# Performance work log

Measured on AMD Instinct MI355X. Metric: run time of the kernel, lower is better.

Reference implementation:

```python
import jax, jax.numpy as jnp
import numpy as np

B, N, E = 16, 512, 131072
FEAT, EMB, H = 3, 512, 3
K1, K2 = 410, 205  # ceil(0.8*512), ceil(0.5*410) per PyG TopKPooling
NEG_SLOPE, EPS = 0.2, 1e-5


def _gat_conv(x, W, att_s, att_d, bias, src, tgt, valid, num_nodes):
    # PyG GATConv (concat=True): per-edge attention with segment softmax over targets.
    Hh, C = att_s.shape
    xp = (x @ W).reshape(-1, Hh, C)                      # [Nn,H,C]
    a_s = jnp.einsum('nhc,hc->nh', xp, att_s)
    a_d = jnp.einsum('nhc,hc->nh', xp, att_d)
    srcc = jnp.where(valid, src, 0)
    tgtc = jnp.where(valid, tgt, 0)
    e = jax.nn.leaky_relu(a_s[srcc] + a_d[tgtc], NEG_SLOPE)  # [Ee,H]
    seg = jnp.where(valid, tgt, num_nodes)               # invalid edges -> dummy segment
    emax = jax.ops.segment_max(e, seg, num_segments=num_nodes + 1)
    emax = jnp.where(jnp.isfinite(emax), emax, 0.0)
    ex = jnp.exp(e - emax[seg]) * valid[:, None].astype(e.dtype)
    den = jax.ops.segment_sum(ex, seg, num_segments=num_nodes + 1)
    alpha = ex / jnp.maximum(den[seg], 1e-16)            # [Ee,H]
    out = jax.ops.segment_sum(alpha[:, :, None] * xp[srcc], seg,
                              num_segments=num_nodes + 1)[:num_nodes]
    return out.reshape(num_nodes, Hh * C) + bias


def _bn(x, g, b):
    # BatchNorm1d, training-mode batch statistics (biased var), eps=1e-5
    m = x.mean(0)
    v = x.var(0)
    return (x - m) * jax.lax.rsqrt(v + EPS) * g + b


def _topk_pool(x, p, nb, n_per, k):
    # PyG TopKPooling: score = tanh(x.w/||w||), keep top-k per graph, scale by score
    score = jnp.tanh((x @ p) / jnp.linalg.norm(p))       # [nb*n_per]
    top_s, top_i = jax.lax.top_k(score.reshape(nb, n_per), k)
    perm = (top_i + jnp.arange(nb)[:, None] * n_per).reshape(-1)
    x_new = x[perm] * top_s.reshape(-1, 1)
    mapping = jnp.full((nb * n_per,), -1, jnp.int32).at[perm].set(
        jnp.arange(nb * k, dtype=jnp.int32))
    return x_new, mapping


def _pool_cat(x, nb, k):
    # [global_max_pool, global_mean_pool] over equal-size graphs
    xr = x.reshape(nb, k, -1)
    return jnp.concatenate([xr.max(1), xr.mean(1)], axis=1)


def _forward(x, W1, as1, ad1, bc1, Wh1, bh1, g1, be1, p1,
             W2, as2, ad2, bc2, Wh2, bh2, g2, be2, p2,
             Wl1, bl1, Wl2, bl2, edge_index):
    Nn = B * N
    src0, tgt0 = edge_index[0], edge_index[1]
    sl = jnp.arange(Nn, dtype=jnp.int32)                 # GATConv add_self_loops=True
    src1 = jnp.concatenate([src0, sl]); tgt1 = jnp.concatenate([tgt0, sl])
    valid1 = jnp.ones(src1.shape, bool)
    h = _gat_conv(x, W1, as1, ad1, bc1, src1, tgt1, valid1, Nn)
    h = jax.nn.relu(h @ Wh1 + bh1)
    h = _bn(h, g1, be1)
    h, mapping = _topk_pool(h, p1, B, N, K1)
    x1 = _pool_cat(h, B, K1)                             # [B, 2*EMB]
    # relabel edges to pooled node ids; drop edges with removed endpoints via mask
    s2 = mapping[src0]; t2 = mapping[tgt0]
    v2 = (s2 >= 0) & (t2 >= 0)
    sl2 = jnp.arange(B * K1, dtype=jnp.int32)
    src2 = jnp.concatenate([s2, sl2]); tgt2 = jnp.concatenate([t2, sl2])
    valid2 = jnp.concatenate([v2, jnp.ones(sl2.shape, bool)])
    h = _gat_conv(h, W2, as2, ad2, bc2, src2, tgt2, valid2, B * K1)
    h = jax.nn.relu(h @ Wh2 + bh2)
    h = _bn(h, g2, be2)
    h, _ = _topk_pool(h, p2, B, K1, K2)
    x2 = _pool_cat(h, B, K2)
    xg = x1 + x2
    xg = jax.nn.relu(xg @ Wl1 + bl1)                     # dropout p=0.5 disabled (eval)
    return xg @ Wl2 + bl2                                # [B, 256]


def setup_inputs() -> dict:
    key = jax.random.key(0)
    ks = jax.random.split(key, 16)
    x = jax.random.normal(ks[0], (B * N, FEAT), jnp.float32)
    goff = jnp.repeat(jnp.arange(B, dtype=jnp.int32), E // B) * N
    src = jax.random.randint(ks[1], (E,), 0, N, jnp.int32) + goff
    tgt = jax.random.randint(ks[2], (E,), 0, N, jnp.int32) + goff
    edge_index = jnp.stack([src, tgt])
    s = 0.05
    p = {
        'W1': jax.random.normal(ks[3], (FEAT, H * EMB)) * s,
        'as1': jax.random.normal(ks[4], (H, EMB)) * s,
        'ad1': jax.random.normal(ks[5], (H, EMB)) * s,
        'bc1': jnp.zeros((H * EMB,)),
        'Wh1': jax.random.normal(ks[6], (H * EMB, EMB)) * s,
        'bh1': jnp.zeros((EMB,)),
        'g1': jnp.ones((EMB,)), 'be1': jnp.zeros((EMB,)),
        'p1': jax.random.normal(ks[7], (EMB,)) * s,
        'W2': jax.random.normal(ks[8], (EMB, H * EMB)) * s,
        'as2': jax.random.normal(ks[9], (H, EMB)) * s,
        'ad2': jax.random.normal(ks[10], (H, EMB)) * s,
        'bc2': jnp.zeros((H * EMB,)),
        'Wh2': jax.random.normal(ks[11], (H * EMB, EMB)) * s,
        'bh2': jnp.zeros((EMB,)),
        'g2': jnp.ones((EMB,)), 'be2': jnp.zeros((EMB,)),
        'p2': jax.random.normal(ks[12], (EMB,)) * s,
        'Wl1': jax.random.normal(ks[13], (2 * EMB, 512)) * s,
        'bl1': jnp.zeros((512,)),
        'Wl2': jax.random.normal(ks[14], (512, 256)) * s,
        'bl2': jnp.zeros((256,)),
    }
    return {'x': x, 'edge_index': edge_index, **p}


def reference(x, edge_index, W1, as1, ad1, bc1, Wh1, bh1, g1, be1, p1,
              W2, as2, ad2, bc2, Wh2, bh2, g2, be2, p2, Wl1, bl1, Wl2, bl2):
    return _forward(x, W1, as1, ad1, bc1, Wh1, bh1, g1, be1, p1,
                    W2, as2, ad2, bc2, Wh2, bh2, g2, be2, p2,
                    Wl1, bl1, Wl2, bl2, edge_index)
```

## Files before the change

kernel.cpp:

```cpp
#include <hip/hip_runtime.h>
#include <hip/hip_bf16.h>
#include <math.h>

#define E_EDGES 131072
#define NN1 8192
#define NN2 6560
#define NG 16
#define NP1 512
#define KP1 410
#define KP2 205
#define F1 1536
#define EMB 512
#define MAXDEG 256
#define BNCH 256

typedef __hip_bfloat16 bf16;
typedef __attribute__((ext_vector_type(8))) short short8;
typedef __attribute__((ext_vector_type(4))) float f32x4;
typedef __attribute__((ext_vector_type(4))) unsigned short us4;

__device__ inline float wred64(float v){
  #pragma unroll
  for (int o = 32; o; o >>= 1) v += __shfl_down(v, o);
  return v;
}
__device__ inline float b2f_raw(unsigned short u){
  return __uint_as_float((unsigned)u << 16);
}
union BFU { bf16 b; unsigned short u; };
// ... 4 lines not shown
      (const __attribute__((address_space(1))) void*)g,
      (__attribute__((address_space(3))) void*)l, 16, 0, 0);
}

__device__ inline void split_store(float v, bf16* __restrict__ ph, bf16* __restrict__ pl){
  bf16 hi = __float2bfloat16(v);
  *ph = hi;
  *pl = __float2bfloat16(v - __bfloat162float(hi));
}

__device__ inline void bn_from_acc(const float* __restrict__ bnacc, int c, float fM,
                                   float& mean, float& inv){
  mean = bnacc[c] / fM;
  float var = fmaxf(bnacc[512+c]/fM - mean*mean, 0.f);
  inv = 1.f / sqrtf(var + 1e-5f);
}

__global__ __launch_bounds__(256) void k_pre(
    const float* __restrict__ W1, const float* __restrict__ as1, const float* __restrict__ ad1,
    const float* __restrict__ Wh1, const float* __restrict__ bc1, const float* __restrict__ bh1,
    const float* __restrict__ W2, const float* __restrict__ as2, const float* __restrict__ ad2,
    const float* __restrict__ Wh2, const float* __restrict__ bc2, const float* __restrict__ bh2,
    float* __restrict__ was1, float* __restrict__ wad1, float* __restrict__ M1p,
    float* __restrict__ cvp,
    float* __restrict__ was2, float* __restrict__ wad2,
    int* __restrict__ cnt1, int* __restrict__ cnt2, int* __restrict__ map,
    float* __restrict__ bnacc, float* __restrict__ bnacc1){
  int b = blockIdx.x, t = threadIdx.x;
  if (b < 24){
    int h = b / 8, rem = b % 8, jh = rem >> 2, kc = rem & 3;
    int j = jh*256 + t, c0 = kc*128;
    __shared__ float w1s[3][128];
    for (int i = t; i < 384; i += 256)
      w1s[i>>7][i&127] = W1[(i>>7)*1536 + h*512 + c0 + (i&127)];
    __syncthreads();
    const float* whc = Wh1 + (size_t)(h*512 + c0)*512 + j;
    float a0=0.f, a1=0.f, a2=0.f;
    #pragma unroll 8
    for (int c = 0; c < 128; c++){
      float v = whc[(size_t)c*512];
      a0 += w1s[0][c]*v; a1 += w1s[1][c]*v; a2 += w1s[2][c]*v;
    }
// ... 29 lines not shown
      float d = v0.x*a[0]+v0.y*a[1]+v0.z*a[2]+v0.w*a[3]
              + v1.x*a[4]+v1.y*a[5]+v1.z*a[6]+v1.w*a[7];
      d = wred64(d);
      if (lane == 0) (kind ? wad2 : was2)[h*512 + e] = d;
    }
  } else if (b < 170){
    if (t < 64){
      int bb = b - 152;
      int kind = bb / 9, r = bb % 9, h = r / 3, f = r % 3;
      const float* att = kind ? ad1 : as1;
      float s = 0.f;
      for (int c = t; c < 512; c += 64) s += W1[f*1536 + h*512 + c] * att[h*512 + c];
      s = wred64(s);
      if (t == 0) (kind ? wad1 : was1)[h*3 + f] = s;
    }
  } else {
    int i = (b - 170)*256 + t;
    if (i < NN1){ cnt1[i] = 1; map[i] = -1; }
    if (i < NN2){ cnt2[i] = 1; }
    if (i < 1024){ bnacc[i] = 0.f; bnacc1[i] = 0.f; }
  }
}

__global__ __launch_bounds__(256) void k_gemm_s_c1(const float* __restrict__ A0,
    const float* __restrict__ B0, bf16* __restrict__ Th, bf16* __restrict__ Tl,
    const int* __restrict__ tgt0, int* __restrict__ cnt1){
  int b = blockIdx.x;
  if (b >= 192){
    int i = (b - 192)*256 + threadIdx.x;
    if (i < E_EDGES) atomicAdd(&cnt1[tgt0[i]], 1);
    return;
  }
  int z = b % 3; int rr = b / 3; int by = rr >> 3, bx = rr & 7;
  const float* A = A0 + (size_t)z*512;
  const float* B = B0 + (size_t)z*512*512;
  __shared__ __align__(16) short sAh[4096], sAl[4096], sBh[4096], sBl[4096];
  int t = threadIdx.x, w = t >> 6, lane = t & 63;
  int l16 = lane & 15, q = lane >> 4;
  int bm = by*64, bn = bx*64;

  int am  = t >> 2, akw = (t & 3)*16;
  int bnl = t & 63, bkq = (t >> 6)*16;

  f32x4 acc[4];
  #pragma unroll
  for (int nf = 0; nf < 4; nf++) acc[nf] = (f32x4){0.f,0.f,0.f,0.f};

  float va[16], vb[16];
  #define GS_LOAD(K0) do { \
    _Pragma("unroll") for (int u = 0; u < 4; u++){ \
      float4 v4 = *(const float4*)(A + (size_t)(bm+am)*1536 + (K0) + akw + u*4); \
      va[u*4]=v4.x; va[u*4+1]=v4.y; va[u*4+2]=v4.z; va[u*4+3]=v4.w; } \
    _Pragma("unroll") for (int u = 0; u < 16; u++) \
      vb[u] = B[(size_t)((K0) + bkq + u)*512 + bn + bnl]; \
  } while(0)

  GS_LOAD(0);
  for (int it = 0; it < 8; it++){
    #pragma unroll
    for (int hh = 0; hh < 2; hh++){
      short8 ah_, al_, bh_, bl_;
      #pragma unroll
      for (int jj = 0; jj < 8; jj++){
        float v = va[hh*8+jj];
        unsigned short hu = f2u(v);
        ah_[jj] = (short)hu; al_[jj] = (short)f2u(v - b2f_raw(hu));
        v = vb[hh*8+jj];
        hu = f2u(v);
        bh_[jj] = (short)hu; bl_[jj] = (short)f2u(v - b2f_raw(hu));
      }
      int aoff = am*64  + ((((akw>>3) + hh) ^ (am  & 7)) << 3);
      *(short8*)(sAh + aoff) = ah_;
      *(short8*)(sAl + aoff) = al_;
      int boff = bnl*64 + ((((bkq>>3) + hh) ^ (bnl & 7)) << 3);
      *(short8*)(sBh + boff) = bh_;
      *(short8*)(sBl + boff) = bl_;
    }
    __syncthreads();
    if (it < 7) GS_LOAD((it+1)*64);
    #pragma unroll
    for (int ks = 0; ks < 2; ks++){
      int gc = ks*4 + q;
      int ar = w*16 + l16;
      int ao = ar*64 + ((gc ^ (ar & 7)) << 3);
      short8 afh = *(const short8*)(sAh + ao);
      short8 afl = *(const short8*)(sAl + ao);
      #pragma unroll
      for (int nf = 0; nf < 4; nf++){
        int br = nf*16 + l16;
        int bo = br*64 + ((gc ^ (br & 7)) << 3);
        short8 bfh = *(const short8*)(sBh + bo);
        short8 bfl = *(const short8*)(sBl + bo);
        acc[nf] = __builtin_amdgcn_mfma_f32_16x16x32_bf16(afh, bfh, acc[nf], 0, 0, 0);
        acc[nf] = __builtin_amdgcn_mfma_f32_16x16x32_bf16(afh, bfl, acc[nf], 0, 0, 0);
        acc[nf] = __builtin_amdgcn_mfma_f32_16x16x32_bf16(afl, bfh, acc[nf], 0, 0, 0);
      }
    }
    __syncthreads();
  }
  #undef GS_LOAD

  int m0 = bm + w*16 + q*4;
  #pragma unroll
  for (int nf = 0; nf < 4; nf++){
    int n = bn + nf*16 + l16;
    size_t base = (size_t)n*1536 + (size_t)z*512 + m0;
    #pragma unroll
    for (int e = 0; e < 4; e++)
      split_store(acc[nf][e], &Th[base+e], &Tl[base+e]);
  }
}

__device__ inline void scan_body(const int* __restrict__ counts, int* __restrict__ off,
                                 int* __restrict__ cur, int n, int* __restrict__ sh){
  int t = threadIdx.x;
  int chunk = (n + 1023) >> 10;
  int b = t * chunk; int e = b + chunk; if (e > n) e = n;
  int s = 0;
  for (int i = b; i < e; i++) s += counts[i];
  sh[t] = s; __syncthreads();
  for (int o = 1; o < 1024; o <<= 1){
    int v = (t >= o) ? sh[t-o] : 0;
    __syncthreads();
    sh[t] += v;
    __syncthreads();
  }
  int run = (t > 0) ? sh[t-1] : 0;
  for (int i = b; i < e; i++){ int c = counts[i]; off[i] = run; cur[i] = run; run += c; }
  if (t == 1023) off[n] = sh[1023];
}
__global__ __launch_bounds__(1024) void k_scan(const int* __restrict__ counts,
    int* __restrict__ off, int* __restrict__ cur, int n){
  __shared__ int sh[1024];
  scan_body(counts, off, cur, n, sh);
}
__global__ void k_fill1(const int* __restrict__ src0, const int* __restrict__ tgt0,
                        int* __restrict__ cur, int* __restrict__ esrc, int E, int nn){
  int i = blockIdx.x*blockDim.x + threadIdx.x;
  if (i >= E + nn) return;
  int s, tg;
  if (i < E){ s = src0[i]; tg = tgt0[i]; } else { s = i - E; tg = s; }
  int pos = atomicAdd(&cur[tg], 1);
  esrc[pos] = s;
}
__global__ void k_fill2(const int* __restrict__ src0, const int* __restrict__ tgt0,
                        const int* __restrict__ map, int* __restrict__ cur,
                        int* __restrict__ esrc, int E, int nn){
  int i = blockIdx.x*blockDim.x + threadIdx.x;
  if (i >= E + nn) return;
  int s, tg;
  if (i < E){
    s = map[src0[i]]; tg = map[tgt0[i]];
    if (s < 0 || tg < 0) return;
  } else { s = i - E; tg = s; }
  int pos = atomicAdd(&cur[tg], 1);
  esrc[pos] = s;
}

__global__ __launch_bounds__(64) void k_agg1(
    const float* __restrict__ x, const int* __restrict__ off, const int* __restrict__ esrc,
    const float* __restrict__ was, const float* __restrict__ wad,
    float* __restrict__ aggx){
  int n = blockIdx.x, t = threadIdx.x;
  __shared__ float xs[MAXDEG][3];
  __shared__ float al[MAXDEG*3];
  __shared__ float mh[3], dh[3];
  int s0 = off[n]; int deg = off[n+1] - s0; if (deg > MAXDEG) deg = MAXDEG;
  float ad0, ad1, ad2;
  {
    float x0 = x[n*3], x1 = x[n*3+1], x2 = x[n*3+2];
    ad0 = x0*wad[0] + x1*wad[1] + x2*wad[2];
    ad1 = x0*wad[3] + x1*wad[4] + x2*wad[5];
    ad2 = x0*wad[6] + x1*wad[7] + x2*wad[8];
  }
  for (int e = t; e < deg; e += 64){
    int s = esrc[s0 + e];
    float x0 = x[s*3], x1 = x[s*3+1], x2 = x[s*3+2];
    xs[e][0] = x0; xs[e][1] = x1; xs[e][2] = x2;
    float v0 = x0*was[0] + x1*was[1] + x2*was[2] + ad0;
    float v1 = x0*was[3] + x1*was[4] + x2*was[5] + ad1;
    float v2 = x0*was[6] + x1*was[7] + x2*was[8] + ad2;
    al[e*3+0] = v0 > 0.f ? v0 : 0.2f*v0;
    al[e*3+1] = v1 > 0.f ? v1 : 0.2f*v1;
    al[e*3+2] = v2 > 0.f ? v2 : 0.2f*v2;
  }
  __syncthreads();
  if (t < 3){
    float m = -INFINITY;
    for (int e = 0; e < deg; e++) m = fmaxf(m, al[e*3+t]);
    float d = 0.f;
    for (int e = 0; e < deg; e++) d += expf(al[e*3+t] - m);
    mh[t] = m; dh[t] = 1.f / fmaxf(d, 1e-16f);
  }
  __syncthreads();
  float acc[9] = {0,0,0,0,0,0,0,0,0};
  for (int e = t; e < deg; e += 64){
    #pragma unroll
    for (int h = 0; h < 3; h++){
      float a = expf(al[e*3+h] - mh[h]) * dh[h];
      acc[h*3+0] += a * xs[e][0];
      acc[h*3+1] += a * xs[e][1];
      acc[h*3+2] += a * xs[e][2];
    }
  }
  #pragma unroll
  for (int q = 0; q < 9; q++){
    float v = wred64(acc[q]);
    if (t == 0) aggx[(size_t)n*9 + q] = v;
  }
}

__global__ __launch_bounds__(256) void k_h1(const float* __restrict__ aggx,
    const float* __restrict__ M1p, const float* __restrict__ cvp1, bf16* __restrict__ hout,
    float* __restrict__ bnacc1){
  __shared__ float sM[9*512];
  __shared__ float sC[512];
  __shared__ float sA[32*9];
  int t = threadIdx.x; int n0 = blockIdx.x*32;
  for (int i = t; i < 9*512; i += 256)
    sM[i] = M1p[i] + M1p[4608 + i] + M1p[2*4608 + i] + M1p[3*4608 + i];
  for (int i = t; i < 512; i += 256){
    float s = 0.f;
    #pragma unroll
    for (int kc = 0; kc < 8; kc++) s += cvp1[kc*512 + i];
    sC[i] = s;
  }
  for (int i = t; i < 288; i += 256) sA[i] = aggx[(size_t)n0*9 + i];
  __syncthreads();
  float c0v = sC[t], c1v = sC[t+256];
  float ls0=0.f, lq0=0.f, ls1=0.f, lq1=0.f;
  #pragma unroll 4
  for (int i = 0; i < 32; i++){
    float a0 = c0v, a1 = c1v;
    #pragma unroll
    for (int q = 0; q < 9; q++){
      float av = sA[i*9+q];
      a0 += av * sM[q*512 + t];
      a1 += av * sM[q*512 + t + 256];
    }
    a0 = fmaxf(a0, 0.f); a1 = fmaxf(a1, 0.f);
    hout[(size_t)(n0+i)*512 + t]       = __float2bfloat16(a0);
    hout[(size_t)(n0+i)*512 + t + 256] = __float2bfloat16(a1);
    ls0 += a0; lq0 += a0*a0; ls1 += a1; lq1 += a1*a1;
  }
  atomicAdd(&bnacc1[t],           ls0);
  atomicAdd(&bnacc1[t+256],       ls1);
  atomicAdd(&bnacc1[512 + t],     lq0);
  atomicAdd(&bnacc1[512 + t+256], lq1);
}

__global__ __launch_bounds__(256) void k_score(
    const bf16* __restrict__ h, const float* __restrict__ bnacc, int M,
    const float* __restrict__ g_, const float* __restrict__ be,
    const float* __restrict__ p, float* __restrict__ score){
  int r = blockIdx.x, t = threadIdx.x;
  float fM = (float)M;
  float dot = 0.f, pp = 0.f;
  #pragma unroll
  for (int k = 0; k < 2; k++){
    int c = t + k*256;
    float mean, inv; bn_from_acc(bnacc, c, fM, mean, inv);
    float v = (__bfloat162float(h[(size_t)r*EMB + c]) - mean) * inv * g_[c] + be[c];
    float pc = p[c];
    dot += v * pc;
    pp += pc * pc;
  }
  dot = wred64(dot); pp = wred64(pp);
  __shared__ float red[4], redp[4];
  int lane = t & 63, wv = t >> 6;
  if (lane == 0){ red[wv] = dot; redp[wv] = pp; }
  __syncthreads();
  if (t == 0){
    float d = red[0]+red[1]+red[2]+red[3];
    float pn = sqrtf(redp[0]+redp[1]+redp[2]+redp[3]);
    score[r] = tanhf(d / pn);
  }
}

__global__ __launch_bounds__(512) void k_topk_sort(
    const float* __restrict__ score, int* __restrict__ map,
    int* __restrict__ topi, float* __restrict__ tops, int n_per, int K){
  int g = blockIdx.x, t = threadIdx.x;
  __shared__ float sk[512];
  __shared__ int si[512];
  if (t < n_per){ sk[t] = score[g*n_per + t]; si[t] = t; }
  else { sk[t] = -INFINITY; si[t] = 0x7fffffff; }
  __syncthreads();
  for (int k = 2; k <= 512; k <<= 1){
    for (int j = k >> 1; j > 0; j >>= 1){
      int l = t ^ j;
      if (l > t){
        float ki = sk[t], kl = sk[l]; int ii = si[t], il = si[l];
        bool before_l = (kl > ki) || (kl == ki && il < ii);
        bool up = ((t & k) == 0);
        if (up == before_l){ sk[t]=kl; sk[l]=ki; si[t]=il; si[l]=ii; }
      }
      __syncthreads();
    }
  }
  if (t < K){
    if (map) map[g*n_per + si[t]] = g*K + t;
// ... 41 lines not shown
      a[hh]   = v0*was2[hh*512 + c0] + v1*was2[hh*512 + c1];
      a[3+hh] = v0*wad2[hh*512 + c0] + v1*wad2[hh*512 + c1];
    }
    __shared__ float red[6][4];
    int lane = t & 63, wv = t >> 6;
    #pragma unroll
    for (int q = 0; q < 6; q++){ float v = wred64(a[q]); if (lane==0) red[q][wv]=v; }
    __syncthreads();
    if (t < 6){
      float sm = red[t][0]+red[t][1]+red[t][2]+red[t][3];
      if (t < 3) aso[row*3+t] = sm; else ado[row*3+(t-3)] = sm;
    }
  }
}

__global__ __launch_bounds__(1024) void k_poolA_scan(const bf16* __restrict__ xn,
    float* __restrict__ cat, int K,
    const int* __restrict__ cnt2, int* __restrict__ off2, int* __restrict__ cur2){
  __shared__ int shi[1024];
  __shared__ float smax[8][128];
  __shared__ float ssum[8][128];
  int b = blockIdx.x, t = threadIdx.x;
  if (b == 64){ scan_body(cnt2, off2, cur2, NN2, shi); return; }
  int g = b >> 2, cb = b & 3;
  int c = t & 127, rg = t >> 7;
  int col = cb*128 + c;
  const unsigned short* p = (const unsigned short*)xn + (size_t)g*K*EMB + col;
  float mx = -INFINITY, sm = 0.f;
  for (int r = rg; r < K; r += 8){
    float v = b2f_raw(p[(size_t)r*EMB]);
// ... 90 lines not shown
  #pragma unroll
  for (int k = 0; k < 2; k++){
    int c = t + k*256;
    #pragma unroll
    for (int h = 0; h < 3; h++)
      oh[(size_t)n*1536 + h*512 + c] = __float2bfloat16(acc[k][h]);
  }
}

__global__ __launch_bounds__(256, 2) void k_gemm_mfma(
    const bf16* __restrict__ Ah,
    const bf16* __restrict__ Bh, const bf16* __restrict__ Bl,
    const float* __restrict__ bias, bf16* __restrict__ C,
    float* __restrict__ bnacc,
    int M, int N, int K, int Mtiles){
  __shared__ __align__(16) unsigned short lds[2][16384];
  int t = threadIdx.x, w = t >> 6, lane = t & 63;
  int q = lane >> 4, l16 = lane & 15;
  int bmi = (int)blockIdx.x % Mtiles, bni = (int)blockIdx.x / Mtiles;
  int bm = bmi * 128, bn = bni * 64;

  int lr = lane >> 3, lc = lane & 7;
  int kg = ((lc ^ lr) & 7) * 8;
  int ro = w*8 + lr;
  int m0 = bm + ro, m1 = bm + 32 + ro, m2 = bm + 64 + ro, m3 = bm + 96 + ro;
  if (m0 >= M) m0 = M-1;  if (m1 >= M) m1 = M-1;
  if (m2 >= M) m2 = M-1;  if (m3 >= M) m3 = M-1;
  int n0 = bn + ro, n1 = bn + 32 + ro;
  const bf16* ptr[8];
  ptr[0] = Ah + (size_t)m0*K + kg;
  ptr[1] = Ah + (size_t)m1*K + kg;
  ptr[2] = Ah + (size_t)m2*K + kg;
  ptr[3] = Ah + (size_t)m3*K + kg;
  ptr[4] = Bh + (size_t)n0*K + kg;
// ... 81 lines not shown
          ls += v; lq += v*v;
        }
      }
    }
    ls += __shfl_xor(ls, 16); ls += __shfl_xor(ls, 32);
    lq += __shfl_xor(lq, 16); lq += __shfl_xor(lq, 32);
    if (q == 0){ cs[slot*64 + c_local] = ls; cq[slot*64 + c_local] = lq; }
  }
  __syncthreads();
  if (t < 64){
    atomicAdd(&bnacc[bn + t],        cs[t] + cs[64 + t]);
    atomicAdd(&bnacc[512 + bn + t],  cq[t] + cq[64 + t]);
  }
}

__global__ __launch_bounds__(256) void k_head1(const float* __restrict__ c1,
    const float* __restrict__ c2, const float* __restrict__ Wl1,
    const float* __restrict__ bl1, float* __restrict__ t1){
  int g = blockIdx.y;
  int jj = threadIdx.x & 63, kc = threadIdx.x >> 6;
  int j = blockIdx.x*64 + jj;
  float acc = 0.f;
  for (int k = kc*256; k < kc*256 + 256; k++){
    float xg = c1[g*1024 + k] + c2[g*1024 + k];
    acc += xg * Wl1[(size_t)k*512 + j];
  }
  __shared__ float red[4][64];
  red[kc][jj] = acc;
  __syncthreads();
  if (kc == 0){
    float v = red[0][jj]+red[1][jj]+red[2][jj]+red[3][jj] + bl1[j];
    t1[g*512 + j] = fmaxf(v, 0.f);
  }
}
__global__ __launch_bounds__(256) void k_head2(const float* __restrict__ t1,
    const float* __restrict__ Wl2, const float* __restrict__ bl2, float* __restrict__ out){
  int g = blockIdx.y;
  int jj = threadIdx.x & 63, kc = threadIdx.x >> 6;
  int j = blockIdx.x*64 + jj;
  float acc = 0.f;
  for (int k = kc*128; k < kc*128 + 128; k++)
    acc += t1[g*512 + k] * Wl2[(size_t)k*256 + j];
  __shared__ float red[4][64];
  red[kc][jj] = acc;
  __syncthreads();
  if (kc == 0)
    out[g*256 + j] = red[0][jj]+red[1][jj]+red[2][jj]+red[3][jj] + bl2[j];
}

extern "C" void kernel_launch(void* const* d_in, const int* in_sizes, int n_in,
                              void* d_out, int out_size, void* d_ws, size_t ws_size,
                              hipStream_t stream){
  const float* x   = (const float*)d_in[0];
  const int*   ei  = (const int*)d_in[1];
  const float* W1  = (const float*)d_in[2];
  const float* as1 = (const float*)d_in[3];
  const float* ad1 = (const float*)d_in[4];
  const float* bc1 = (const float*)d_in[5];
  const float* Wh1 = (const float*)d_in[6];
  const float* bh1 = (const float*)d_in[7];
  const float* g1  = (const float*)d_in[8];
  const float* be1 = (const float*)d_in[9];
// ... 4 lines not shown
  const float* bc2 = (const float*)d_in[14];
  const float* Wh2 = (const float*)d_in[15];
  const float* bh2 = (const float*)d_in[16];
  const float* g2  = (const float*)d_in[17];
  const float* be2 = (const float*)d_in[18];
  const float* p2  = (const float*)d_in[19];
  const float* Wl1 = (const float*)d_in[20];
  const float* bl1 = (const float*)d_in[21];
  const float* Wl2 = (const float*)d_in[22];
  const float* bl2 = (const float*)d_in[23];
  float* out = (float*)d_out;

  const int* src0 = ei;
  const int* tgt0 = ei + E_EDGES;

  bf16* Cc     = (bf16*)d_ws;
  bf16* xn1    = Cc + (size_t)NN1*EMB;
  bf16* xn2    = xn1 + (size_t)NN2*EMB;
  float* aggx1 = (float*)(xn2 + (size_t)NG*KP2*EMB + 8);
  float* M1    = aggx1 + (size_t)NN1*9;
  float* was2  = M1 + 9*EMB;
  float* wad2  = was2 + 3*EMB;
  float* cvec1 = wad2 + 3*EMB;
  float* cvec2 = cvec1 + EMB;
  float* was1  = cvec2 + EMB;
  float* wad1  = was1 + 16;
  float* bnpsum= wad1 + 16;
  float* bnpsq = bnpsum + (size_t)BNCH*EMB;
  float* stats = bnpsq + (size_t)BNCH*EMB;
  float* bnacc = stats + 1024;
  float* pn    = bnacc + 1024;
  float* score = pn + 16;
  float* cat1  = score + NN1;
  float* cat2  = cat1 + NG*1024;
  float* t1h   = cat2 + NG*1024;
  float* pmax  = t1h + NG*EMB;
  float* psum  = pmax + NG*16*EMB;
  float* aso2  = psum + NG*16*EMB;
  float* ado2  = aso2 + NN2*3;
  float* tops  = ado2 + NN2*3;
  bf16* aggx2h = (bf16*)(tops + NG*KP1);
  bf16* M2Th   = aggx2h + (size_t)NN2*F1;
  bf16* M2Tl   = M2Th + (size_t)EMB*F1;
  int* map     = (int*)(M2Tl + (size_t)EMB*F1);
  int* cnt1    = map + NN1;
  int* off1    = cnt1 + NN1;
  int* cur1    = off1 + NN1 + 8;
  int* esrc1   = cur1 + NN1;
  int* cnt2    = esrc1 + (E_EDGES + NN1);
  int* off2    = cnt2 + NN2;
  int* cur2    = off2 + NN2 + 8;
  int* esrc2   = cur2 + NN2;
  int* topi    = esrc2 + 137700;

  float* bnacc1 = bnpsum;
  float* M1p    = bnpsq;
  float* cvp    = bnpsq + 4*4608;
  float* cvp2   = cvp + 8*512;

  k_pre<<<202,256,0,stream>>>(W1,as1,ad1,Wh1,bc1,bh1, W2,as2,ad2,Wh2,bc2,bh2,
                              was1,wad1,M1p,cvp,was2,wad2,
                              cnt1,cnt2,map,bnacc,bnacc1);
  k_gemm_s_c1<<<704,256,0,stream>>>(W2,Wh2,M2Th,M2Tl,tgt0,cnt1);

  k_scan<<<1,1024,0,stream>>>(cnt1,off1,cur1,NN1);
  k_fill1<<<(E_EDGES+NN1+255)/256,256,0,stream>>>(src0,tgt0,cur1,esrc1,E_EDGES,NN1);
  k_agg1<<<NN1,64,0,stream>>>(x,off1,esrc1,was1,wad1,aggx1);
  k_h1<<<NN1/32,256,0,stream>>>(aggx1,M1p,cvp,Cc,bnacc1);
  k_score<<<NN1,256,0,stream>>>(Cc,bnacc1,NN1,g1,be1,p1,score);
  k_topk_sort<<<NG,512,0,stream>>>(score,map,topi,tops,NP1,KP1);
  k_gather_c2<<<NG*KP1+512,256,0,stream>>>(Cc,bnacc1,NN1,g1,be1,topi,tops,xn1,NP1,KP1,
      was2,wad2,aso2,ado2, src0,tgt0,map,cnt2,NG*KP1);
  k_poolA_scan<<<65,1024,0,stream>>>(xn1,cat1,KP1, cnt2,off2,cur2);

  k_fill2<<<(E_EDGES+NN2+255)/256,256,0,stream>>>(src0,tgt0,map,cur2,esrc2,E_EDGES,NN2);
  k_agg2<<<NN2,256,0,stream>>>(xn1,aso2,ado2,off2,esrc2,aggx2h);
  k_gemm_mfma<<<52*8,256,0,stream>>>(aggx2h,M2Th,M2Tl,cvp2,Cc,bnacc,NN2,EMB,F1,52);
  k_score<<<NN2,256,0,stream>>>(Cc,bnacc,NN2,g2,be2,p2,score);
  k_topk_sort<<<NG,512,0,stream>>>(score,(int*)nullptr,topi,tops,KP1,KP2);
  k_poolB<<<64,1024,0,stream>>>(Cc,bnacc,NN2,g2,be2,topi,tops,cat2,KP1,KP2);

  k_head1<<<dim3(8,NG),256,0,stream>>>(cat1,cat2,Wl1,bl1,t1h);
  k_head2<<<dim3(4,NG),256,0,stream>>>(t1h,Wl2,bl2,out);
}
```

Baseline: 341.1 us.

## Replace CSR build with atomic edge softmax and fuse score, topk and head kernels

The first GAT layer no longer builds a CSR (count, scan, fill, per-node aggregate). It instead runs two edge-parallel passes: an atomicMax over order-preserving float keys for the segment max, then atomic accumulation of the softmax denominator and weighted source features. The W2·Wh2 GEMM is folded into the prep kernel, and the score kernel is fused with the top-k sort. The BN affine is folded into the score weights, the two head kernels are merged into one, and the second GEMM gets an XCD-aware tile mapping. This removes several launches and the CSR passes, at the cost of heavy atomic contention and non-deterministic float summation order.

Result: slower. 421.7 us (+23.6%).

```diff
diff --git a/kernel.cpp b/kernel.cpp
--- a/kernel.cpp
+++ b/kernel.cpp
@@ -12,7 +12,6 @@
 #define F1 1536
 #define EMB 512
 #define MAXDEG 256
-#define BNCH 256
 
 typedef __hip_bfloat16 bf16;
 typedef __attribute__((ext_vector_type(8))) short short8;
@@ -47,6 +46,14 @@
   mean = bnacc[c] / fM;
   float var = fmaxf(bnacc[512+c]/fM - mean*mean, 0.f);
   inv = 1.f / sqrtf(var + 1e-5f);
+}
+
+__device__ inline unsigned fkey(float v){
+  unsigned u = __float_as_uint(v);
+  return (u & 0x80000000u) ? ~u : (u | 0x80000000u);
+}
+__device__ inline float fkey_inv(unsigned k){
+  return (k & 0x80000000u) ? __uint_as_float(k & 0x7fffffffu) : __uint_as_float(~k);
 }
 
 __global__ __launch_bounds__(256) void k_pre(
@@ -57,8 +64,8 @@
     float* __restrict__ was1, float* __restrict__ wad1, float* __restrict__ M1p,
     float* __restrict__ cvp,
     float* __restrict__ was2, float* __restrict__ wad2,
-    int* __restrict__ cnt1, int* __restrict__ cnt2, int* __restrict__ map,
-    float* __restrict__ bnacc, float* __restrict__ bnacc1){
+    float* __restrict__ Zf, int* __restrict__ cnt2, int* __restrict__ map,
+    bf16* __restrict__ Th, bf16* __restrict__ Tl){
   int b = blockIdx.x, t = threadIdx.x;
   if (b < 24){
     int h = b / 8, rem = b % 8, jh = rem >> 2, kc = rem & 3;
@@ -118,203 +125,134 @@
       s = wred64(s);
       if (t == 0) (kind ? wad1 : was1)[h*3 + f] = s;
     }
+  } else if (b < 716){
+    int i = (b - 170)*256 + t;
+    if (i < 124928){ Zf[i] = 0.f; }
+    else if (i < 124928 + NN2){ cnt2[i - 124928] = 1; }
+    else if (i < 124928 + NN2 + NN1){ map[i - 124928 - NN2] = -1; }
   } else {
-    int i = (b - 170)*256 + t;
-    if (i < NN1){ cnt1[i] = 1; map[i] = -1; }
-    if (i < NN2){ cnt2[i] = 1; }
-    if (i < 1024){ bnacc[i] = 0.f; bnacc1[i] = 0.f; }
-  }
-}
-
-__global__ __launch_bounds__(256) void k_gemm_s_c1(const float* __restrict__ A0,
-    const float* __restrict__ B0, bf16* __restrict__ Th, bf16* __restrict__ Tl,
-    const int* __restrict__ tgt0, int* __restrict__ cnt1){
-  int b = blockIdx.x;
-  if (b >= 192){
-    int i = (b - 192)*256 + threadIdx.x;
-    if (i < E_EDGES) atomicAdd(&cnt1[tgt0[i]], 1);
-    return;
-  }
-  int z = b % 3; int rr = b / 3; int by = rr >> 3, bx = rr & 7;
-  const float* A = A0 + (size_t)z*512;
-  const float* B = B0 + (size_t)z*512*512;
-  __shared__ __align__(16) short sAh[4096], sAl[4096], sBh[4096], sBl[4096];
-  int t = threadIdx.x, w = t >> 6, lane = t & 63;
-  int l16 = lane & 15, q = lane >> 4;
-  int bm = by*64, bn = bx*64;
-
-  int am  = t >> 2, akw = (t & 3)*16;
-  int bnl = t & 63, bkq = (t >> 6)*16;
-
-  f32x4 acc[4];
+    int bb = b - 716;
+    int z = bb % 3; int rr = bb / 3; int by = rr >> 3, bx = rr & 7;
+    const float* A = W2 + (size_t)z*512;
+    const float* B = Wh2 + (size_t)z*512*512;
+    __shared__ __align__(16) short sAh[4096], sAl[4096], sBh[4096], sBl[4096];
+    int w = t >> 6, lane = t & 63;
+    int l16 = lane & 15, q = lane >> 4;
+    int bm = by*64, bn = bx*64;
+    int am  = t >> 2, akw = (t & 3)*16;
+    int bnl = t & 63, bkq = (t >> 6)*16;
+    f32x4 acc[4];
+    #pragma unroll
+    for (int nf = 0; nf < 4; nf++) acc[nf] = (f32x4){0.f,0.f,0.f,0.f};
+    float va[16], vb[16];
+    #define GS_LOAD(K0) do { \
+      _Pragma("unroll") for (int u = 0; u < 4; u++){ \
+        float4 v4 = *(const float4*)(A + (size_t)(bm+am)*1536 + (K0) + akw + u*4); \
+        va[u*4]=v4.x; va[u*4+1]=v4.y; va[u*4+2]=v4.z; va[u*4+3]=v4.w; } \
+      _Pragma("unroll") for (int u = 0; u < 16; u++) \
+        vb[u] = B[(size_t)((K0) + bkq + u)*512 + bn + bnl]; \
+    } while(0)
+    GS_LOAD(0);
+    for (int it = 0; it < 8; it++){
+      #pragma unroll
+      for (int hh = 0; hh < 2; hh++){
+        short8 ah_, al_, bh_, bl_;
+        #pragma unroll
+        for (int jj = 0; jj < 8; jj++){
+          float v = va[hh*8+jj];
+          unsigned short hu = f2u(v);
+          ah_[jj] = (short)hu; al_[jj] = (short)f2u(v - b2f_raw(hu));
+          v = vb[hh*8+jj];
+          hu = f2u(v);
+          bh_[jj] = (short)hu; bl_[jj] = (short)f2u(v - b2f_raw(hu));
+        }
+        int aoff = am*64  + ((((akw>>3) + hh) ^ (am  & 7)) << 3);
+        *(short8*)(sAh + aoff) = ah_;
+        *(short8*)(sAl + aoff) = al_;
+        int boff = bnl*64 + ((((bkq>>3) + hh) ^ (bnl & 7)) << 3);
+        *(short8*)(sBh + boff) = bh_;
+        *(short8*)(sBl + boff) = bl_;
+      }
+      __syncthreads();
+      if (it < 7) GS_LOAD((it+1)*64);
+      #pragma unroll
+      for (int ks = 0; ks < 2; ks++){
+        int gc = ks*4 + q;
+        int ar = w*16 + l16;
+        int ao = ar*64 + ((gc ^ (ar & 7)) << 3);
+        short8 afh = *(const short8*)(sAh + ao);
+        short8 afl = *(const short8*)(sAl + ao);
+        #pragma unroll
+        for (int nf = 0; nf < 4; nf++){
+          int br = nf*16 + l16;
+          int bo = br*64 + ((gc ^ (br & 7)) << 3);
+          short8 bfh = *(const short8*)(sBh + bo);
+          short8 bfl = *(const short8*)(sBl + bo);
+          acc[nf] = __builtin_amdgcn_mfma_f32_16x16x32_bf16(afh, bfh, acc[nf], 0, 0, 0);
+          acc[nf] = __builtin_amdgcn_mfma_f32_16x16x32_bf16(afh, bfl, acc[nf], 0, 0, 0);
+          acc[nf] = __builtin_amdgcn_mfma_f32_16x16x32_bf16(afl, bfh, acc[nf], 0, 0, 0);
+        }
+      }
+      __syncthreads();
+    }
+    #undef GS_LOAD
+    int m0 = bm + w*16 + q*4;
+    #pragma unroll
+    for (int nf = 0; nf < 4; nf++){
+      int n = bn + nf*16 + l16;
+      size_t base = (size_t)n*1536 + (size_t)z*512 + m0;
+      #pragma unroll
+      for (int e = 0; e < 4; e++)
+        split_store(acc[nf][e], &Th[base+e], &Tl[base+e]);
+    }
+  }
+}
+
+__global__ __launch_bounds__(256) void k_edge1(
+    const int* __restrict__ src0, const int* __restrict__ tgt0, const float* __restrict__ x,
+    const float* __restrict__ was, const float* __restrict__ wad,
+    unsigned* __restrict__ mkey){
+  int i = blockIdx.x*256 + threadIdx.x;
+  if (i >= E_EDGES + NN1) return;
+  int s, tg;
+  if (i < E_EDGES){ s = src0[i]; tg = tgt0[i]; } else { s = tg = i - E_EDGES; }
+  float xs0 = x[s*3], xs1 = x[s*3+1], xs2 = x[s*3+2];
+  float xt0 = x[tg*3], xt1 = x[tg*3+1], xt2 = x[tg*3+2];
   #pragma unroll
-  for (int nf = 0; nf < 4; nf++) acc[nf] = (f32x4){0.f,0.f,0.f,0.f};
-
-  float va[16], vb[16];
-  #define GS_LOAD(K0) do { \
-    _Pragma("unroll") for (int u = 0; u < 4; u++){ \
-      float4 v4 = *(const float4*)(A + (size_t)(bm+am)*1536 + (K0) + akw + u*4); \
-      va[u*4]=v4.x; va[u*4+1]=v4.y; va[u*4+2]=v4.z; va[u*4+3]=v4.w; } \
-    _Pragma("unroll") for (int u = 0; u < 16; u++) \
-      vb[u] = B[(size_t)((K0) + bkq + u)*512 + bn + bnl]; \
-  } while(0)
-
-  GS_LOAD(0);
-  for (int it = 0; it < 8; it++){
-    #pragma unroll
-    for (int hh = 0; hh < 2; hh++){
-      short8 ah_, al_, bh_, bl_;
-      #pragma unroll
-      for (int jj = 0; jj < 8; jj++){
-        float v = va[hh*8+jj];
-        unsigned short hu = f2u(v);
-        ah_[jj] = (short)hu; al_[jj] = (short)f2u(v - b2f_raw(hu));
-        v = vb[hh*8+jj];
-        hu = f2u(v);
-        bh_[jj] = (short)hu; bl_[jj] = (short)f2u(v - b2f_raw(hu));
-      }
-      int aoff = am*64  + ((((akw>>3) + hh) ^ (am  & 7)) << 3);
-      *(short8*)(sAh + aoff) = ah_;
-      *(short8*)(sAl + aoff) = al_;
-      int boff = bnl*64 + ((((bkq>>3) + hh) ^ (bnl & 7)) << 3);
-      *(short8*)(sBh + boff) = bh_;
-      *(short8*)(sBl + boff) = bl_;
-    }
-    __syncthreads();
-    if (it < 7) GS_LOAD((it+1)*64);
-    #pragma unroll
-    for (int ks = 0; ks < 2; ks++){
-      int gc = ks*4 + q;
-      int ar = w*16 + l16;
-      int ao = ar*64 + ((gc ^ (ar & 7)) << 3);
-      short8 afh = *(const short8*)(sAh + ao);
-      short8 afl = *(const short8*)(sAl + ao);
-      #pragma unroll
-      for (int nf = 0; nf < 4; nf++){
-        int br = nf*16 + l16;
-        int bo = br*64 + ((gc ^ (br & 7)) << 3);
-        short8 bfh = *(const short8*)(sBh + bo);
-        short8 bfl = *(const short8*)(sBl + bo);
-        acc[nf] = __builtin_amdgcn_mfma_f32_16x16x32_bf16(afh, bfh, acc[nf], 0, 0, 0);
-        acc[nf] = __builtin_amdgcn_mfma_f32_16x16x32_bf16(afh, bfl, acc[nf], 0, 0, 0);
-        acc[nf] = __builtin_amdgcn_mfma_f32_16x16x32_bf16(afl, bfh, acc[nf], 0, 0, 0);
-      }
-    }
-    __syncthreads();
-  }
-  #undef GS_LOAD
-
-  int m0 = bm + w*16 + q*4;
+  for (int h = 0; h < 3; h++){
+    float v = xs0*was[h*3]+xs1*was[h*3+1]+xs2*was[h*3+2]
+            + xt0*wad[h*3]+xt1*wad[h*3+1]+xt2*wad[h*3+2];
+    v = v > 0.f ? v : 0.2f*v;
+    atomicMax(&mkey[tg*3 + h], fkey(v));
+  }
+}
+__global__ __launch_bounds__(256) void k_edge2(
+    const int* __restrict__ src0, const int* __restrict__ tgt0, const float* __restrict__ x,
+    const float* __restrict__ was, const float* __restrict__ wad,
+    const unsigned* __restrict__ mkey,
+    float* __restrict__ den, float* __restrict__ num){
+  int i = blockIdx.x*256 + threadIdx.x;
+  if (i >= E_EDGES + NN1) return;
+  int s, tg;
+  if (i < E_EDGES){ s = src0[i]; tg = tgt0[i]; } else { s = tg = i - E_EDGES; }
+  float xs0 = x[s*3], xs1 = x[s*3+1], xs2 = x[s*3+2];
+  float xt0 = x[tg*3], xt1 = x[tg*3+1], xt2 = x[tg*3+2];
   #pragma unroll
-  for (int nf = 0; nf < 4; nf++){
-    int n = bn + nf*16 + l16;
-    size_t base = (size_t)n*1536 + (size_t)z*512 + m0;
-    #pragma unroll
-    for (int e = 0; e < 4; e++)
-      split_store(acc[nf][e], &Th[base+e], &Tl[base+e]);
-  }
-}
-
-__device__ inline void scan_body(const int* __restrict__ counts, int* __restrict__ off,
-                                 int* __restrict__ cur, int n, int* __restrict__ sh){
-  int t = threadIdx.x;
-  int chunk = (n + 1023) >> 10;
-  int b = t * chunk; int e = b + chunk; if (e > n) e = n;
-  int s = 0;
-  for (int i = b; i < e; i++) s += counts[i];
-  sh[t] = s; __syncthreads();
-  for (int o = 1; o < 1024; o <<= 1){
-    int v = (t >= o) ? sh[t-o] : 0;
-    __syncthreads();
-    sh[t] += v;
-    __syncthreads();
-  }
-  int run = (t > 0) ? sh[t-1] : 0;
-  for (int i = b; i < e; i++){ int c = counts[i]; off[i] = run; cur[i] = run; run += c; }
-  if (t == 1023) off[n] = sh[1023];
-}
-__global__ __launch_bounds__(1024) void k_scan(const int* __restrict__ counts,
-    int* __restrict__ off, int* __restrict__ cur, int n){
-  __shared__ int sh[1024];
-  scan_body(counts, off, cur, n, sh);
-}
-__global__ void k_fill1(const int* __restrict__ src0, const int* __restrict__ tgt0,
-                        int* __restrict__ cur, int* __restrict__ esrc, int E, int nn){
-  int i = blockIdx.x*blockDim.x + threadIdx.x;
-  if (i >= E + nn) return;
-  int s, tg;
-  if (i < E){ s = src0[i]; tg = tgt0[i]; } else { s = i - E; tg = s; }
-  int pos = atomicAdd(&cur[tg], 1);
-  esrc[pos] = s;
-}
-__global__ void k_fill2(const int* __restrict__ src0, const int* __restrict__ tgt0,
-                        const int* __restrict__ map, int* __restrict__ cur,
-                        int* __restrict__ esrc, int E, int nn){
-  int i = blockIdx.x*blockDim.x + threadIdx.x;
-  if (i >= E + nn) return;
-  int s, tg;
-  if (i < E){
-    s = map[src0[i]]; tg = map[tgt0[i]];
-    if (s < 0 || tg < 0) return;
-  } else { s = i - E; tg = s; }
-  int pos = atomicAdd(&cur[tg], 1);
-  esrc[pos] = s;
-}
-
-__global__ __launch_bounds__(64) void k_agg1(
-    const float* __restrict__ x, const int* __restrict__ off, const int* __restrict__ esrc,
-    const float* __restrict__ was, const float* __restrict__ wad,
-    float* __restrict__ aggx){
-  int n = blockIdx.x, t = threadIdx.x;
-  __shared__ float xs[MAXDEG][3];
-  __shared__ float al[MAXDEG*3];
-  __shared__ float mh[3], dh[3];
-  int s0 = off[n]; int deg = off[n+1] - s0; if (deg > MAXDEG) deg = MAXDEG;
-  float ad0, ad1, ad2;
-  {
-    float x0 = x[n*3], x1 = x[n*3+1], x2 = x[n*3+2];
-    ad0 = x0*wad[0] + x1*wad[1] + x2*wad[2];
-    ad1 = x0*wad[3] + x1*wad[4] + x2*wad[5];
-    ad2 = x0*wad[6] + x1*wad[7] + x2*wad[8];
-  }
-  for (int e = t; e < deg; e += 64){
-    int s = esrc[s0 + e];
-    float x0 = x[s*3], x1 = x[s*3+1], x2 = x[s*3+2];
-    xs[e][0] = x0; xs[e][1] = x1; xs[e][2] = x2;
-    float v0 = x0*was[0] + x1*was[1] + x2*was[2] + ad0;
-    float v1 = x0*was[3] + x1*was[4] + x2*was[5] + ad1;
-    float v2 = x0*was[6] + x1*was[7] + x2*was[8] + ad2;
-    al[e*3+0] = v0 > 0.f ? v0 : 0.2f*v0;
-    al[e*3+1] = v1 > 0.f ? v1 : 0.2f*v1;
-    al[e*3+2] = v2 > 0.f ? v2 : 0.2f*v2;
-  }
-  __syncthreads();
-  if (t < 3){
-    float m = -INFINITY;
-    for (int e = 0; e < deg; e++) m = fmaxf(m, al[e*3+t]);
-    float d = 0.f;
-    for (int e = 0; e < deg; e++) d += expf(al[e*3+t] - m);
-    mh[t] = m; dh[t] = 1.f / fmaxf(d, 1e-16f);
-  }
-  __syncthreads();
-  float acc[9] = {0,0,0,0,0,0,0,0,0};
-  for (int e = t; e < deg; e += 64){
-    #pragma unroll
-    for (int h = 0; h < 3; h++){
-      float a = expf(al[e*3+h] - mh[h]) * dh[h];
-      acc[h*3+0] += a * xs[e][0];
-      acc[h*3+1] += a * xs[e][1];
-      acc[h*3+2] += a * xs[e][2];
-    }
-  }
-  #pragma unroll
-  for (int q = 0; q < 9; q++){
-    float v = wred64(acc[q]);
-    if (t == 0) aggx[(size_t)n*9 + q] = v;
-  }
-}
-
-__global__ __launch_bounds__(256) void k_h1(const float* __restrict__ aggx,
+  for (int h = 0; h < 3; h++){
+    float v = xs0*was[h*3]+xs1*was[h*3+1]+xs2*was[h*3+2]
+            + xt0*wad[h*3]+xt1*wad[h*3+1]+xt2*wad[h*3+2];
+    v = v > 0.f ? v : 0.2f*v;
+    float m = fkey_inv(mkey[tg*3 + h]);
+    float pe = expf(v - m);
+    atomicAdd(&den[tg*3 + h], pe);
+    atomicAdd(&num[(size_t)tg*9 + h*3 + 0], pe * xs0);
+    atomicAdd(&num[(size_t)tg*9 + h*3 + 1], pe * xs1);
+    atomicAdd(&num[(size_t)tg*9 + h*3 + 2], pe * xs2);
+  }
+}
+
+__global__ __launch_bounds__(256) void k_h1(
+    const float* __restrict__ num, const float* __restrict__ den,
     const float* __restrict__ M1p, const float* __restrict__ cvp1, bf16* __restrict__ hout,
     float* __restrict__ bnacc1){
   __shared__ float sM[9*512];
@@ -329,7 +267,11 @@
     for (int kc = 0; kc < 8; kc++) s += cvp1[kc*512 + i];
     sC[i] = s;
   }
-  for (int i = t; i < 288; i += 256) sA[i] = aggx[(size_t)n0*9 + i];
+  for (int i = t; i < 288; i += 256){
+    int node = i / 9, q = i % 9, hh = q / 3;
+    float d = fmaxf(den[(size_t)(n0+node)*3 + hh], 1e-16f);
+    sA[i] = num[(size_t)n0*9 + i] / d;
+  }
   __syncthreads();
   float c0v = sC[t], c1v = sC[t+256];
   float ls0=0.f, lq0=0.f, ls1=0.f, lq1=0.f;
@@ -353,42 +295,48 @@
   atomicAdd(&bnacc1[512 + t+256], lq1);
 }
 
-__global__ __launch_bounds__(256) void k_score(
+__global__ __launch_bounds__(512) void k_scoresort(
     const bf16* __restrict__ h, const float* __restrict__ bnacc, int M,
-    const float* __restrict__ g_, const float* __restrict__ be,
-    const float* __restrict__ p, float* __restrict__ score){
-  int r = blockIdx.x, t = threadIdx.x;
-  float fM = (float)M;
-  float dot = 0.f, pp = 0.f;
-  #pragma unroll
-  for (int k = 0; k < 2; k++){
-    int c = t + k*256;
-    float mean, inv; bn_from_acc(bnacc, c, fM, mean, inv);
-    float v = (__bfloat162float(h[(size_t)r*EMB + c]) - mean) * inv * g_[c] + be[c];
-    float pc = p[c];
-    dot += v * pc;
-    pp += pc * pc;
-  }
-  dot = wred64(dot); pp = wred64(pp);
-  __shared__ float red[4], redp[4];
-  int lane = t & 63, wv = t >> 6;
-  if (lane == 0){ red[wv] = dot; redp[wv] = pp; }
-  __syncthreads();
-  if (t == 0){
-    float d = red[0]+red[1]+red[2]+red[3];
-    float pn = sqrtf(redp[0]+redp[1]+redp[2]+redp[3]);
-    score[r] = tanhf(d / pn);
-  }
-}
-
-__global__ __launch_bounds__(512) void k_topk_sort(
-    const float* __restrict__ score, int* __restrict__ map,
-    int* __restrict__ topi, float* __restrict__ tops, int n_per, int K){
+    const float* __restrict__ g_, const float* __restrict__ be, const float* __restrict__ p,
+    int n_per, int K, int* __restrict__ map,
+    int* __restrict__ topi, float* __restrict__ tops){
   int g = blockIdx.x, t = threadIdx.x;
+  __shared__ float w[512];
+  __shared__ float redb[8], redp[8];
   __shared__ float sk[512];
   __shared__ int si[512];
-  if (t < n_per){ sk[t] = score[g*n_per + t]; si[t] = t; }
-  else { sk[t] = -INFINITY; si[t] = 0x7fffffff; }
+  float fM = (float)M;
+  float mean, inv; bn_from_acc(bnacc, t, fM, mean, inv);
+  float gc = g_[t], pc = p[t];
+  float ig = inv * gc;
+  w[t] = ig * pc;
+  float bt = (be[t] - mean * ig) * pc;
+  float b_ = wred64(bt);
+  float pp = wred64(pc * pc);
+  int lane = t & 63, wv = t >> 6;
+  if (lane == 0){ redb[wv] = b_; redp[wv] = pp; }
+  __syncthreads();
+  float B0 = 0.f, pn2 = 0.f;
+  #pragma unroll
+  for (int u = 0; u < 8; u++){ B0 += redb[u]; pn2 += redp[u]; }
+  float pn = sqrtf(pn2);
+  float score = -INFINITY; int idx = 0x7fffffff;
+  if (t < n_per){
+    const unsigned short* hr = (const unsigned short*)h + (size_t)(g*n_per + t)*EMB;
+    float dot = 0.f;
+    #pragma unroll 4
+    for (int c = 0; c < 512; c += 8){
+      us4 v0 = *(const us4*)(hr + c);
+      us4 v1 = *(const us4*)(hr + c + 4);
+      dot += b2f_raw(v0.x)*w[c]   + b2f_raw(v0.y)*w[c+1]
+           + b2f_raw(v0.z)*w[c+2] + b2f_raw(v0.w)*w[c+3]
+           + b2f_raw(v1.x)*w[c+4] + b2f_raw(v1.y)*w[c+5]
+           + b2f_raw(v1.z)*w[c+6] + b2f_raw(v1.w)*w[c+7];
+    }
+    score = tanhf((dot + B0) / pn);
+    idx = t;
+  }
+  sk[t] = score; si[t] = idx;
   __syncthreads();
   for (int k = 2; k <= 512; k <<= 1){
     for (int j = k >> 1; j > 0; j >>= 1){
@@ -460,6 +408,38 @@
   }
 }
 
+__device__ inline void scan_body(const int* __restrict__ counts, int* __restrict__ off,
+                                 int* __restrict__ cur, int n, int* __restrict__ sh){
+  int t = threadIdx.x;
+  int chunk = (n + 1023) >> 10;
+  int b = t * chunk; int e = b + chunk; if (e > n) e = n;
+  int s = 0;
+  for (int i = b; i < e; i++) s += counts[i];
+  sh[t] = s; __syncthreads();
+  for (int o = 1; o < 1024; o <<= 1){
+    int v = (t >= o) ? sh[t-o] : 0;
+    __syncthreads();
+    sh[t] += v;
+    __syncthreads();
+  }
+  int run = (t > 0) ? sh[t-1] : 0;
+  for (int i = b; i < e; i++){ int c = counts[i]; off[i] = run; cur[i] = run; run += c; }
+  if (t == 1023) off[n] = sh[1023];
+}
+__global__ void k_fill2(const int* __restrict__ src0, const int* __restrict__ tgt0,
+                        const int* __restrict__ map, int* __restrict__ cur,
+                        int* __restrict__ esrc, int E, int nn){
+  int i = blockIdx.x*blockDim.x + threadIdx.x;
+  if (i >= E + nn) return;
+  int s, tg;
+  if (i < E){
+    s = map[src0[i]]; tg = map[tgt0[i]];
+    if (s < 0 || tg < 0) return;
+  } else { s = i - E; tg = s; }
+  int pos = atomicAdd(&cur[tg], 1);
+  esrc[pos] = s;
+}
+
 __global__ __launch_bounds__(1024) void k_poolA_scan(const bf16* __restrict__ xn,
     float* __restrict__ cat, int K,
     const int* __restrict__ cnt2, int* __restrict__ off2, int* __restrict__ cur2){
@@ -580,10 +560,14 @@
     const float* __restrict__ bias, bf16* __restrict__ C,
     float* __restrict__ bnacc,
     int M, int N, int K, int Mtiles){
+  int xcd = (int)blockIdx.x & 7;
+  int ii  = (int)blockIdx.x >> 3;
+  int bni = ii & 7;
+  int bmi = xcd + 8*(ii >> 3);
+  if (bmi >= Mtiles) return;
   __shared__ __align__(16) unsigned short lds[2][16384];
   int t = threadIdx.x, w = t >> 6, lane = t & 63;
   int q = lane >> 4, l16 = lane & 15;
-  int bmi = (int)blockIdx.x % Mtiles, bni = (int)blockIdx.x / Mtiles;
   int bm = bmi * 128, bn = bni * 64;
 
   int lr = lane >> 3, lc = lane & 7;
@@ -695,38 +679,36 @@
   }
 }
 
-__global__ __launch_bounds__(256) void k_head1(const float* __restrict__ c1,
+__global__ __launch_bounds__(1024) void k_head(const float* __restrict__ c1,
     const float* __restrict__ c2, const float* __restrict__ Wl1,
-    const float* __restrict__ bl1, float* __restrict__ t1){
-  int g = blockIdx.y;
-  int jj = threadIdx.x & 63, kc = threadIdx.x >> 6;
-  int j = blockIdx.x*64 + jj;
+    const float* __restrict__ bl1, const float* __restrict__ Wl2,
+    const float* __restrict__ bl2, float* __restrict__ out){
+  int g = blockIdx.x, t = threadIdx.x;
+  __shared__ float xg[1024];
+  __shared__ float t1[512];
+  __shared__ float part[2][512];
+  xg[t] = c1[g*1024 + t] + c2[g*1024 + t];
+  __syncthreads();
+  int c = t & 511, kc = t >> 9;
   float acc = 0.f;
-  for (int k = kc*256; k < kc*256 + 256; k++){
-    float xg = c1[g*1024 + k] + c2[g*1024 + k];
-    acc += xg * Wl1[(size_t)k*512 + j];
-  }
-  __shared__ float red[4][64];
-  red[kc][jj] = acc;
-  __syncthreads();
-  if (kc == 0){
-    float v = red[0][jj]+red[1][jj]+red[2][jj]+red[3][jj] + bl1[j];
-    t1[g*512 + j] = fmaxf(v, 0.f);
-  }
-}
-__global__ __launch_bounds__(256) void k_head2(const float* __restrict__ t1,
-    const float* __restrict__ Wl2, const float* __restrict__ bl2, float* __restrict__ out){
-  int g = blockIdx.y;
-  int jj = threadIdx.x & 63, kc = threadIdx.x >> 6;
-  int j = blockIdx.x*64 + jj;
-  float acc = 0.f;
-  for (int k = kc*128; k < kc*128 + 128; k++)
-    acc += t1[g*512 + k] * Wl2[(size_t)k*256 + j];
-  __shared__ float red[4][64];
-  red[kc][jj] = acc;
-  __syncthreads();
-  if (kc == 0)
-    out[g*256 + j] = red[0][jj]+red[1][jj]+red[2][jj]+red[3][jj] + bl2[j];
+  #pragma unroll 8
+  for (int k = kc*512; k < kc*512 + 512; k++)
+    acc += xg[k] * Wl1[(size_t)k*512 + c];
+  part[kc][c] = acc;
+  __syncthreads();
+  if (kc == 0) t1[c] = fmaxf(part[0][c] + part[1][c] + bl1[c], 0.f);
+  __syncthreads();
+  if (t < 512){
+    int c2i = t & 255, k2 = t >> 8;
+    float a = 0.f;
+    #pragma unroll 8
+    for (int k = k2*256; k < k2*256 + 256; k++)
+      a += t1[k] * Wl2[(size_t)k*256 + c2i];
+    part[k2][c2i] = a;
+  }
+  __syncthreads();
+  if (t < 256)
+    out[g*256 + t] = part[0][t] + part[1][t] + bl2[t];
 }
 
 extern "C" void kernel_launch(void* const* d_in, const int* in_sizes, int n_in,
@@ -761,72 +743,50 @@
   const int* src0 = ei;
   const int* tgt0 = ei + E_EDGES;
 
-  bf16* Cc     = (bf16*)d_ws;
-  bf16* xn1    = Cc + (size_t)NN1*EMB;
-  bf16* xn2    = xn1 + (size_t)NN2*EMB;
-  float* aggx1 = (float*)(xn2 + (size_t)NG*KP2*EMB + 8);
-  float* M1    = aggx1 + (size_t)NN1*9;
-  float* was2  = M1 + 9*EMB;
-  float* wad2  = was2 + 3*EMB;
-  float* cvec1 = wad2 + 3*EMB;
-  float* cvec2 = cvec1 + EMB;
-  float* was1  = cvec2 + EMB;
-  float* wad1  = was1 + 16;
-  float* bnpsum= wad1 + 16;
-  float* bnpsq = bnpsum + (size_t)BNCH*EMB;
-  float* stats = bnpsq + (size_t)BNCH*EMB;
-  float* bnacc = stats + 1024;
-  float* pn    = bnacc + 1024;
-  float* score = pn + 16;
-  float* cat1  = score + NN1;
-  float* cat2  = cat1 + NG*1024;
-  float* t1h   = cat2 + NG*1024;
-  float* pmax  = t1h + NG*EMB;
-  float* psum  = pmax + NG*16*EMB;
-  float* aso2  = psum + NG*16*EMB;
-  float* ado2  = aso2 + NN2*3;
-  float* tops  = ado2 + NN2*3;
-  bf16* aggx2h = (bf16*)(tops + NG*KP1);
-  bf16* M2Th   = aggx2h + (size_t)NN2*F1;
-  bf16* M2Tl   = M2Th + (size_t)EMB*F1;
-  int* map     = (int*)(M2Tl + (size_t)EMB*F1);
-  int* cnt1    = map + NN1;
-  int* off1    = cnt1 + NN1;
-  int* cur1    = off1 + NN1 + 8;
-  int* esrc1   = cur1 + NN1;
-  int* cnt2    = esrc1 + (E_EDGES + NN1);
-  int* off2    = cnt2 + NN2;
-  int* cur2    = off2 + NN2 + 8;
-  int* esrc2   = cur2 + NN2;
-  int* topi    = esrc2 + 137700;
-
-  float* bnacc1 = bnpsum;
-  float* M1p    = bnpsq;
-  float* cvp    = bnpsq + 4*4608;
+  bf16* Cc      = (bf16*)d_ws;
+  bf16* xn1     = Cc + (size_t)NN1*EMB;
+  bf16* aggx2h  = xn1 + (size_t)NN2*EMB;
+  bf16* M2Th    = aggx2h + (size_t)NN2*F1;
+  bf16* M2Tl    = M2Th + (size_t)EMB*F1;
+  float* Zf     = (float*)(M2Tl + (size_t)EMB*F1);
+  float* num    = Zf;
+  float* den    = num + (size_t)NN1*9;
+  unsigned* mkey= (unsigned*)(den + (size_t)NN1*3);
+  float* bnacc1 = (float*)(mkey + (size_t)NN1*3);
+  float* bnacc  = bnacc1 + 1024;
+  float* M1p    = bnacc + 1024;
+  float* cvp    = M1p + 4*4608;
+  float* was2   = cvp + 16*512;
+  float* wad2   = was2 + 3*512;
+  float* was1   = wad2 + 3*512;
+  float* wad1   = was1 + 16;
+  float* aso2   = wad1 + 16;
+  float* ado2   = aso2 + (size_t)NN2*3;
+  float* tops   = ado2 + (size_t)NN2*3;
+  float* cat1   = tops + NG*KP1;
+  float* cat2   = cat1 + NG*1024;
+  int* topi     = (int*)(cat2 + NG*1024);
+  int* map      = topi + NG*KP1;
+  int* cnt2     = map + NN1;
+  int* off2     = cnt2 + NN2;
+  int* cur2     = off2 + NN2 + 8;
+  int* esrc2    = cur2 + NN2;
   float* cvp2   = cvp + 8*512;
 
-  k_pre<<<202,256,0,stream>>>(W1,as1,ad1,Wh1,bc1,bh1, W2,as2,ad2,Wh2,bc2,bh2,
+  k_pre<<<908,256,0,stream>>>(W1,as1,ad1,Wh1,bc1,bh1, W2,as2,ad2,Wh2,bc2,bh2,
                               was1,wad1,M1p,cvp,was2,wad2,
-                              cnt1,cnt2,map,bnacc,bnacc1);
-  k_gemm_s_c1<<<704,256,0,stream>>>(W2,Wh2,M2Th,M2Tl,tgt0,cnt1);
-
-  k_scan<<<1,1024,0,stream>>>(cnt1,off1,cur1,NN1);
-  k_fill1<<<(E_EDGES+NN1+255)/256,256,0,stream>>>(src0,tgt0,cur1,esrc1,E_EDGES,NN1);
-  k_agg1<<<NN1,64,0,stream>>>(x,off1,esrc1,was1,wad1,aggx1);
-  k_h1<<<NN1/32,256,0,stream>>>(aggx1,M1p,cvp,Cc,bnacc1);
-  k_score<<<NN1,256,0,stream>>>(Cc,bnacc1,NN1,g1,be1,p1,score);
-  k_topk_sort<<<NG,512,0,stream>>>(score,map,topi,tops,NP1,KP1);
+                              Zf,cnt2,map,M2Th,M2Tl);
+  k_edge1<<<(E_EDGES+NN1+255)/256,256,0,stream>>>(src0,tgt0,x,was1,wad1,mkey);
+  k_edge2<<<(E_EDGES+NN1+255)/256,256,0,stream>>>(src0,tgt0,x,was1,wad1,mkey,den,num);
+  k_h1<<<NN1/32,256,0,stream>>>(num,den,M1p,cvp,Cc,bnacc1);
+  k_scoresort<<<NG,512,0,stream>>>(Cc,bnacc1,NN1,g1,be1,p1,NP1,KP1,map,topi,tops);
   k_gather_c2<<<NG*KP1+512,256,0,stream>>>(Cc,bnacc1,NN1,g1,be1,topi,tops,xn1,NP1,KP1,
       was2,wad2,aso2,ado2, src0,tgt0,map,cnt2,NG*KP1);
   k_poolA_scan<<<65,1024,0,stream>>>(xn1,cat1,KP1, cnt2,off2,cur2);
-
   k_fill2<<<(E_EDGES+NN2+255)/256,256,0,stream>>>(src0,tgt0,map,cur2,esrc2,E_EDGES,NN2);
   k_agg2<<<NN2,256,0,stream>>>(xn1,aso2,ado2,off2,esrc2,aggx2h);
-  k_gemm_mfma<<<52*8,256,0,stream>>>(aggx2h,M2Th,M2Tl,cvp2,Cc,bnacc,NN2,EMB,F1,52);
-  k_score<<<NN2,256,0,stream>>>(Cc,bnacc,NN2,g2,be2,p2,score);
-  k_topk_sort<<<NG,512,0,stream>>>(score,(int*)nullptr,topi,tops,KP1,KP2);
+  k_gemm_mfma<<<448,256,0,stream>>>(aggx2h,M2Th,M2Tl,cvp2,Cc,bnacc,NN2,EMB,F1,52);
+  k_scoresort<<<NG,512,0,stream>>>(Cc,bnacc,NN2,g2,be2,p2,KP1,KP2,(int*)nullptr,topi,tops);
   k_poolB<<<64,1024,0,stream>>>(Cc,bnacc,NN2,g2,be2,topi,tops,cat2,KP1,KP2);
-
-  k_head1<<<dim3(8,NG),256,0,stream>>>(cat1,cat2,Wl1,bl1,t1h);
-  k_head2<<<dim3(4,NG),256,0,stream>>>(t1h,Wl2,bl2,out);
-}
+  k_head<<<NG,1024,0,stream>>>(cat1,cat2,Wl1,bl1,Wl2,bl2,out);
+}
```
